# Optimization experiments

Measured on AMD Instinct MI355X. Metric: run time of the kernel, lower is better.

Reference implementation:

```python
import jax, jax.numpy as jnp
import numpy as np

B, DIM, H, W = 2, 48, 256, 256
HEADS = 8
CHEAD = DIM // HEADS
HID = int(DIM * 2)


def _conv2d(x, w, stride=1, pad=0, dil=1, groups=1):
    return jax.lax.conv_general_dilated(
        x, w, (stride, stride), [(pad, pad), (pad, pad)],
        rhs_dilation=(dil, dil), feature_group_count=groups,
        dimension_numbers=('NCHW', 'OIHW', 'NCHW'))


def _ln(x, w, b):
    # WithBias LayerNorm over the channel axis (to_3d makes channels the last dim)
    mu = jnp.mean(x, axis=1, keepdims=True)
    var = jnp.mean((x - mu) ** 2, axis=1, keepdims=True)
    return (x - mu) / jnp.sqrt(var + 1e-5) * w[None, :, None, None] + b[None, :, None, None]


def _gelu(x):
    return jax.nn.gelu(x, approximate=False)


def setup_inputs() -> dict:
    key = jax.random.key(0)
    ks = iter(jax.random.split(key, 40))
    nrm = lambda *s: jax.random.normal(next(ks), s, dtype=jnp.float32) * 0.02
    d = dict(
        x=jax.random.normal(next(ks), (B, DIM, H, W), dtype=jnp.float32),
        ln1_w=jnp.ones(DIM), ln1_b=jnp.zeros(DIM),
        qkv_w=nrm(3 * DIM, DIM),            # 1x1x1 Conv3d == channel linear
        qkv_dw_w=nrm(3 * DIM, 1, 3, 3),     # center depth slice of 3x3x3 depthwise (depth=1 input)
        proj_w=nrm(DIM, DIM),
        fc_w=nrm(9, 3 * HEADS), fc_b=jnp.zeros(9),
        dep_w=nrm(DIM, 9, 3, 3), dep_b=jnp.zeros(DIM),  # groups = dim//heads
        l2q_w=nrm(DIM, DIM), l2q_b=jnp.zeros(DIM),
        temperature=jnp.ones(HEADS),
        ln2_w=jnp.ones(DIM), ln2_b=jnp.zeros(DIM),
        pin_w=nrm(3 * HID, DIM),
        dw1_w=nrm(HID, 1, 3, 3), dw2_w=nrm(HID, 1, 3, 3), dw3_w=nrm(HID, 1, 3, 3),
        pout_w=nrm(DIM, HID),
    )
    for i in range(3):
        d[f'cv_w{i}'] = nrm(DIM, DIM, 3, 3)
        d[f'cv_b{i}'] = jnp.zeros(DIM)
        d[f'cln_w{i}'] = jnp.ones(DIM)
        d[f'cln_b{i}'] = jnp.zeros(DIM)
    return d


def _forward(x, ln1_w, ln1_b, qkv_w, qkv_dw_w, proj_w, fc_w, fc_b, dep_w, dep_b,
             l2q_w, l2q_b, temperature, ln2_w, ln2_b, pin_w, dw1_w, dw2_w, dw3_w,
             pout_w, cv_w0, cv_b0, cln_w0, cln_b0, cv_w1, cv_b1, cln_w1, cln_b1,
             cv_w2, cv_b2, cln_w2, cln_b2):
    b, c, h, w = x.shape
    heads = temperature.shape[0]
    chead = c // heads

    # ---- Conv2DTransformer branch -> pooled descriptor x_d [b, c]
    t = x
    for cw, cb, lw, lb in ((cv_w0, cv_b0, cln_w0, cln_b0),
                           (cv_w1, cv_b1, cln_w1, cln_b1),
                           (cv_w2, cv_b2, cln_w2, cln_b2)):
        t = _conv2d(t, cw, stride=2, pad=1) + cb[None, :, None, None]
        t = jax.nn.relu(_ln(t, lw, lb))
        t = jax.lax.reduce_window(t, -jnp.inf, jax.lax.max, (1, 1, 2, 2), (1, 1, 2, 2), 'VALID')
    x_d = _gelu(jnp.mean(t, axis=(2, 3)))  # [b, c]

    # ---- Attention
    xn = _ln(x, ln1_w, ln1_b)
    qkv = jnp.einsum('oc,bchw->bohw', qkv_w, xn)
    qkv = _conv2d(qkv, qkv_dw_w, pad=1, groups=3 * c)  # depthwise, [b,3c,h,w]

    # conv-attention path: raw-memory reshape exactly as torch .reshape
    f_all = qkv.reshape(b, h * w, 3 * heads, chead).transpose(0, 2, 1, 3)  # [b,3H,hw,chead]
    f_all = jnp.einsum('oi,bipc->bopc', fc_w, f_all) + fc_b[None, :, None, None]  # [b,9,hw,chead]
    f_conv = f_all.transpose(0, 3, 1, 2).reshape(b, 9 * chead, h, w)
    out_conv = _conv2d(f_conv, dep_w, pad=1, groups=chead) + dep_b[None, :, None, None]

    # outer-product bias from pooled descriptor
    q0 = (x_d @ l2q_w.T + l2q_b).reshape(b, heads, chead)
    q0m = q0[:, :, :, None] * q0[:, :, None, :]  # [b,head,chead,chead]

    q, k, v = jnp.split(qkv, 3, axis=1)
    rs = lambda t_: t_.reshape(b, heads, chead, h * w)
    q, k, v = rs(q), rs(k), rs(v)
    nz = lambda t_: t_ / jnp.maximum(jnp.linalg.norm(t_, axis=-1, keepdims=True), 1e-12)
    q, k = nz(q), nz(k)

    attn = jnp.einsum('bhcx,bhdx->bhcd', q, k) * temperature[None, :, None, None]
    attn = jax.nn.softmax(attn * q0m, axis=-1)
    out = jnp.einsum('bhcd,bhdx->bhcx', attn, v).reshape(b, c, h, w)
    out = jnp.einsum('oc,bchw->bohw', proj_w, out) + out_conv

    x = x + out

    # ---- FeedForward (3-branch dilated depthwise)
    xn2 = _ln(x, ln2_w, ln2_b)
    y = jnp.einsum('oc,bchw->bohw', pin_w, xn2)  # [b,3*hid,h,w]
    hid = y.shape[1] // 3
    y1, y2, y3 = jnp.split(y, 3, axis=1)
    y1 = _conv2d(y1, dw1_w, pad=1, groups=hid)
    y2 = _conv2d(y2, dw2_w, pad=2, dil=2, groups=hid)
    y3 = _conv2d(y3, dw3_w, pad=3, dil=3, groups=hid)
    y = _gelu(y1) * y2 * y3
    return x + jnp.einsum('oc,bchw->bohw', pout_w, y)


def reference(x, ln1_w, ln1_b, qkv_w, qkv_dw_w, proj_w, fc_w, fc_b, dep_w, dep_b,
              l2q_w, l2q_b, temperature, ln2_w, ln2_b, pin_w, dw1_w, dw2_w, dw3_w,
              pout_w, cv_w0, cv_b0, cln_w0, cln_b0, cv_w1, cv_b1, cln_w1, cln_b1,
              cv_w2, cv_b2, cln_w2, cln_b2):
    return _forward(x, ln1_w, ln1_b, qkv_w, qkv_dw_w, proj_w, fc_w, fc_b, dep_w, dep_b,
                    l2q_w, l2q_b, temperature, ln2_w, ln2_b, pin_w, dw1_w, dw2_w, dw3_w,
                    pout_w, cv_w0, cv_b0, cln_w0, cln_b0, cv_w1, cv_b1, cln_w1, cln_b1,
                    cv_w2, cv_b2, cln_w2, cln_b2)
```

## Files before the change

kernel.cpp:

```cpp
#include <hip/hip_runtime.h>

constexpr int NB = 2;
constexpr int NC = 48;
constexpr int NH = 256;
constexpr int NW = 256;
constexpr int NP = NH * NW;
constexpr int NHEADS = 8;
constexpr int NCHD = 6;
constexpr int NHID = 96;
constexpr int GSEG = 64;

typedef unsigned short bf16_t;
typedef __attribute__((ext_vector_type(8))) short bf16x8;
typedef __attribute__((ext_vector_type(4))) float f32x4;

__device__ __forceinline__ float bf2f(bf16_t u) {
  union { unsigned int i; float f; } c; c.i = ((unsigned int)u) << 16; return c.f;
}
__device__ __forceinline__ bf16_t f2bf(float f) {
  union { float f; unsigned int i; } c; c.f = f;
  unsigned int r = (c.i + 0x7FFFu + ((c.i >> 16) & 1u)) >> 16;
  return (bf16_t)r;
}
__device__ __forceinline__ void unpack2(unsigned int u, float& a, float& b) {
  union { unsigned int i; float f; } c0, c1;
  c0.i = u << 16; c1.i = u & 0xffff0000u;
  a = c0.f; b = c1.f;
}

__device__ __forceinline__ float gelu_f(float v) {
  float u = v * (0.79788456f + 0.0356774081f * v * v);
  u = fminf(fmaxf(u, -9.f), 9.f);
  float e = __expf(-2.f * u);
  float th = (1.f - e) / (1.f + e);
  return 0.5f * v * (1.f + th);
}

#define STENCIL_ROW(LROW, D, WVAL0, WVAL1, WVAL2, ACC)                        \
  {                                                                            \
    const float* lp = &lds[(LROW) * 272 + quad * 4];                           \
    float4 va = *(const float4*)lp;                                            \
    float4 vb = *(const float4*)(lp + 4);                                      \
    float4 vc = *(const float4*)(lp + 8);                                      \
    float v[12] = {va.x, va.y, va.z, va.w, vb.x, vb.y, vb.z, vb.w,             \
                   vc.x, vc.y, vc.z, vc.w};                                    \
    _Pragma("unroll") for (int jj = 0; jj < 4; ++jj) {                         \
      ACC[jj] = fmaf(v[jj - (D) + 4], WVAL0, ACC[jj]);                         \
      ACC[jj] = fmaf(v[jj + 4], WVAL1, ACC[jj]);                               \
      ACC[jj] = fmaf(v[jj + (D) + 4], WVAL2, ACC[jj]);                         \
    }                                                                          \
  }

__global__ __launch_bounds__(512) void k_conv_s2_tile(const float* __restrict__ in,
                                                      const float* __restrict__ w,
                                                      const float* __restrict__ bias,
                                                      float* __restrict__ out,
                                                      int IH, int IW, int OH, int OW) {
  __shared__ float lds[16 * 442];
  int tilesX = OW >> 3;
  int tilesY = OH >> 3;
  int blk = blockIdx.x;
  int tx = blk % tilesX;
  int t = blk / tilesX;
  int ty = t % tilesY;
  int b = t / tilesY;
  int oy0 = ty * 8, ox0 = tx * 8;
  int iy0 = oy0 * 2 - 1, ix0 = ox0 * 2 - 1;
  const float* inb = in + (size_t)b * NC * IH * IW;

  int lane = threadIdx.x & 63;
  int oy = lane >> 3, ox = lane & 7;
  int ocb = __builtin_amdgcn_readfirstlane((threadIdx.x >> 6) * 6);
  float acc[6];
  #pragma unroll
  for (int j = 0; j < 6; ++j) acc[j] = bias[ocb + j];
  int rbase = oy * 52;

  for (int chunk = 0; chunk < 3; ++chunk) {
    int icb = chunk * 16;
    for (int i = threadIdx.x; i < 16 * 17 * 17; i += 512) {
      int cc = i % 17;
      int t2 = i / 17;
      int rr = t2 % 17;
      int ic = t2 / 17;
      float v = 0.f;
      int iy = iy0 + rr, ix = ix0 + cc;
      if ((unsigned)iy < (unsigned)IH && (unsigned)ix < (unsigned)IW)
        v = inb[((size_t)(icb + ic) * IH + iy) * IW + ix];
      lds[ic * 442 + rr * 26 + ((cc & 1) ? 13 + (cc >> 1) : (cc >> 1))] = v;
    }
    __syncthreads();

    for (int ic16 = 0; ic16 < 16; ++ic16) {
      const float* base = lds + ic16 * 442 + rbase;
      float e0[3], e1[3], ov[3];
      #pragma unroll
      for (int ky = 0; ky < 3; ++ky) {
        const float* rowp = base + ky * 26;
        e0[ky] = rowp[ox];
        e1[ky] = rowp[ox + 1];
        ov[ky] = rowp[13 + ox];
      }
      const float* wpc = w + (size_t)(ocb * 48 + icb + ic16) * 9;
      #pragma unroll
      for (int j = 0; j < 6; ++j) {
        const float* wp = wpc + (size_t)j * 48 * 9;
        float a = acc[j];
        #pragma unroll
        for (int ky = 0; ky < 3; ++ky) {
          a = fmaf(wp[ky * 3 + 0], e0[ky], a);
          a = fmaf(wp[ky * 3 + 1], ov[ky], a);
          a = fmaf(wp[ky * 3 + 2], e1[ky], a);
        }
        acc[j] = a;
      }
    }
    __syncthreads();
  }

  float* ob = out + (size_t)b * NC * OH * OW;
  #pragma unroll
  for (int j = 0; j < 6; ++j)
    ob[((size_t)(ocb + j) * OH + oy0 + oy) * OW + ox0 + ox] = acc[j];
}

__global__ void k_lnpool(const float* __restrict__ in, const float* __restrict__ lw,
                         const float* __restrict__ lb, float* __restrict__ out,
                         int IH, int IW) {
  int OH = IH >> 1, OW = IW >> 1;
  int idx = blockIdx.x * blockDim.x + threadIdx.x;
  int total = NB * OH * OW;
  if (idx >= total) return;
  int ox = idx % OW;
  int t = idx / OW;
  int oy = t % OH;
  int b = t / OH;
  const float* inb = in + (size_t)b * NC * IH * IW;
  float mu[4], rs[4];
  #pragma unroll
  for (int q = 0; q < 4; ++q) {
    int iy = oy * 2 + (q >> 1), ix = ox * 2 + (q & 1);
    float s = 0.f, ss = 0.f;
    for (int c = 0; c < NC; ++c) {
      float v = inb[((size_t)c * IH + iy) * IW + ix];
      s += v; ss += v * v;
    }
    float m = s * (1.f / NC);
    mu[q] = m;
    rs[q] = rsqrtf(fmaxf(ss * (1.f / NC) - m * m, 0.f) + 1e-5f);
  }
  for (int c = 0; c < NC; ++c) {
    float best = 0.f;
    float wv = lw[c], bv = lb[c];
    #pragma unroll
    for (int q = 0; q < 4; ++q) {
      int iy = oy * 2 + (q >> 1), ix = ox * 2 + (q & 1);
      float v = inb[((size_t)c * IH + iy) * IW + ix];
      v = (v - mu[q]) * rs[q] * wv + bv;
      best = fmaxf(best, fmaxf(v, 0.f));
    }
    out[((size_t)(b * NC + c) * OH + oy) * OW + ox] = best;
  }
}

__global__ void k_head(const float* __restrict__ p3, const float* __restrict__ l2qw,
                       const float* __restrict__ l2qb, float* __restrict__ q0m) {
  __shared__ float xd[NC], q0[NC];
  int b = blockIdx.x, t = threadIdx.x;
  if (t < NC) {
    float s = 0.f;
    for (int i = 0; i < 16; ++i) s += p3[(b * NC + t) * 16 + i];
    xd[t] = gelu_f(s * (1.f / 16.f));
  }
  __syncthreads();
  if (t < NC) {
    float a = l2qb[t];
    for (int c = 0; c < NC; ++c) a += xd[c] * l2qw[t * NC + c];
    q0[t] = a;
  }
  __syncthreads();
  if (t < NHEADS * NCHD * NCHD) {
    int h = t / 36, r = t % 36, c = r / 6, d = r % 6;
    q0m[b * 288 + t] = q0[h * 6 + c] * q0[h * 6 + d];
  }
}

__global__ void k_prep(const float* __restrict__ qkvw, const float* __restrict__ ln1w,
                       const float* __restrict__ ln1b, const float* __restrict__ pinw,
                       const float* __restrict__ ln2w, const float* __restrict__ ln2b,
                       const float* __restrict__ poutw, const float* __restrict__ projw,
                       float* __restrict__ SB, bf16_t* __restrict__ WA1,
                       bf16_t* __restrict__ WA2, bf16_t* __restrict__ WP,
                       bf16_t* __restrict__ WJ) {
  int t = blockIdx.x * blockDim.x + threadIdx.x;
  int stride = gridDim.x * blockDim.x;
  if (t < 144) {
    float s = 0.f, bb = 0.f;
    for (int c = 0; c < 48; ++c) {
      float w = qkvw[t * 48 + c];
      s = fmaf(w, ln1w[c], s); bb = fmaf(w, ln1b[c], bb);
    }
    SB[t] = s; SB[144 + t] = bb;
  } else if (t < 144 + 288) {
    int o = t - 144;
    float s = 0.f, bb = 0.f;
    for (int c = 0; c < 48; ++c) {
      float w = pinw[o * 48 + c];
      s = fmaf(w, ln2w[c], s); bb = fmaf(w, ln2b[c], bb);
    }
    SB[288 + o] = s; SB[576 + o] = bb;
  }
  for (int i = t; i < 9 * 1024; i += stride) {
    int j = i & 7, lane = (i >> 3) & 63, s = (i >> 9) & 1, ot = i >> 10;
    int o = ot * 16 + (lane & 15);
    int k = s * 32 + ((lane >> 4) << 3) + j;
    float v = (k < 48) ? qkvw[o * 48 + k] * ln1w[k] : 0.f;
    WA1[i] = f2bf(v);
  }
  for (int i = t; i < 18 * 1024; i += stride) {
    int j = i & 7, lane = (i >> 3) & 63, s = (i >> 9) & 1, ot = i >> 10;
    int o = ot * 16 + (lane & 15);
    int k = s * 32 + ((lane >> 4) << 3) + j;
    float v = (k < 48) ? pinw[o * 48 + k] * ln2w[k] : 0.f;
    WA2[i] = f2bf(v);
  }
  for (int i = t; i < 9 * 512; i += stride) {
    int j = i & 7, lane = (i >> 3) & 63;
    int fi = i >> 9;
    int s = fi % 3, ot = fi / 3;
    int o = ot * 16 + (lane & 15);
    int k = s * 32 + ((lane >> 4) << 3) + j;
    WP[i] = f2bf(poutw[o * 96 + k]);
  }
  for (int i = t; i < 6 * 512; i += stride) {
    int j = i & 7, lane = (i >> 3) & 63;
    int fi = i >> 9;
    int s = fi & 1, ot = fi >> 1;
    int o = ot * 16 + (lane & 15);
    int k = s * 32 + ((lane >> 4) << 3) + j;
    float v = (k < 48) ? projw[o * 48 + k] : 0.f;
    WJ[i] = f2bf(v);
  }
}

__global__ __launch_bounds__(256) void k_chmix_mfma(const float* __restrict__ x,
                                                    const bf16_t* __restrict__ WA,
                                                    const float* __restrict__ S,
                                                    const float* __restrict__ Bc,
                                                    bf16_t* __restrict__ out,
                                                    int nout) {
  __shared__ bf16_t xT[64 * 72];
  __shared__ float smu[64], srstd[64];
  int blk = blockIdx.x;
  int pxt = blk & 1023;
  int b = blk >> 10;
  int pbase = pxt * 64;
  const float* xb = x + (size_t)b * NC * NP + pbase;
  int p4 = threadIdx.x & 15, k0 = threadIdx.x >> 4;
  #pragma unroll
  for (int it = 0; it < 3; ++it) {
    int k = k0 + it * 16;
    float4 v = *(const float4*)(xb + (size_t)k * NP + p4 * 4);
    xT[(p4 * 4 + 0) * 72 + k] = f2bf(v.x);
    xT[(p4 * 4 + 1) * 72 + k] = f2bf(v.y);
    xT[(p4 * 4 + 2) * 72 + k] = f2bf(v.z);
    xT[(p4 * 4 + 3) * 72 + k] = f2bf(v.w);
  }
  {
    int k = 48 + k0;
    xT[(p4 * 4 + 0) * 72 + k] = 0;
    xT[(p4 * 4 + 1) * 72 + k] = 0;
    xT[(p4 * 4 + 2) * 72 + k] = 0;
    xT[(p4 * 4 + 3) * 72 + k] = 0;
  }
  __syncthreads();
  if (threadIdx.x < 64) {
    int t = threadIdx.x;
    float s = 0.f, ss = 0.f;
    #pragma unroll
    for (int k4 = 0; k4 < 12; ++k4) {
      ushort4 u = *(const ushort4*)&xT[t * 72 + k4 * 4];
      float a0 = bf2f(u.x), a1 = bf2f(u.y), a2 = bf2f(u.z), a3 = bf2f(u.w);
      s += a0 + a1 + a2 + a3;
      ss = fmaf(a0, a0, ss); ss = fmaf(a1, a1, ss);
      ss = fmaf(a2, a2, ss); ss = fmaf(a3, a3, ss);
    }
    float mu = s * (1.f / NC);
    smu[t] = mu;
    srstd[t] = rsqrtf(fmaxf(ss * (1.f / NC) - mu * mu, 0.f) + 1e-5f);
  }
  int w = threadIdx.x >> 6;
  int lane = threadIdx.x & 63;
  bf16x8 bfr0 = *(const bf16x8*)&xT[(w * 16 + (lane & 15)) * 72 + ((lane >> 4) << 3)];
  bf16x8 bfr1 = *(const bf16x8*)&xT[(w * 16 + (lane & 15)) * 72 + 32 + ((lane >> 4) << 3)];
  __syncthreads();
  float mu = smu[w * 16 + (lane & 15)];
  float rs = srstd[w * 16 + (lane & 15)];
  int p = pbase + w * 16 + (lane & 15);
  int nt = nout >> 4;
  bf16_t* ob = out + (size_t)b * nout * NP + p;
  for (int ot = 0; ot < nt; ++ot) {
    bf16x8 a0 = *(const bf16x8*)(WA + (size_t)(ot * 2 + 0) * 512 + lane * 8);
    bf16x8 a1 = *(const bf16x8*)(WA + (size_t)(ot * 2 + 1) * 512 + lane * 8);
    f32x4 acc = {0.f, 0.f, 0.f, 0.f};
    acc = __builtin_amdgcn_mfma_f32_16x16x32_bf16(a0, bfr0, acc, 0, 0, 0);
    acc = __builtin_amdgcn_mfma_f32_16x16x32_bf16(a1, bfr1, acc, 0, 0, 0);
    int orow = ot * 16 + ((lane >> 4) << 2);
    #pragma unroll
    for (int j = 0; j < 4; ++j) {
      int o = orow + j;
      float r = fmaf(rs, acc[j] - mu * S[o], Bc[o]);
      ob[(size_t)o * NP] = f2bf(r);
    }
  }
}

__global__ __launch_bounds__(256) void k_dw144(const bf16_t* __restrict__ in,
                                               const float* __restrict__ w9,
                                               bf16_t* __restrict__ out) {
  __shared__ float lds[6 * 272];
  int blk = blockIdx.x;
  int rq = blk & 63;
  int ch = (blk >> 6) % 144;
  int b = blk / (144 * 64);
  int yy0 = rq * 4;
  const bf16_t* ib = in + (size_t)(b * 144 + ch) * NP;
  for (int i = threadIdx.x; i < 6 * 68; i += 256) {
    int sr = i / 68, c4 = i % 68;
    int iy = yy0 + sr - 1;
    float4 v = make_float4(0.f, 0.f, 0.f, 0.f);
    if ((unsigned)iy < (unsigned)NH && c4 >= 1 && c4 <= 64) {
      ushort4 u = *(const ushort4*)(ib + iy * NW + (c4 - 1) * 4);
      v = make_float4(bf2f(u.x), bf2f(u.y), bf2f(u.z), bf2f(u.w));
    }
    *(float4*)(&lds[sr * 272 + c4 * 4]) = v;
  }
  __syncthreads();
  int q = threadIdx.x >> 6;
  int quad = threadIdx.x & 63;
  const float* wp = w9 + ch * 9;
  float acc[4] = {0.f, 0.f, 0.f, 0.f};
  #pragma unroll
  for (int rr = 0; rr < 3; ++rr)
    STENCIL_ROW(q + rr, 1, wp[rr * 3 + 0], wp[rr * 3 + 1], wp[rr * 3 + 2], acc);
  *(ushort4*)(out + (size_t)(b * 144 + ch) * NP + (yy0 + q) * NW + quad * 4) =
      make_ushort4(f2bf(acc[0]), f2bf(acc[1]), f2bf(acc[2]), f2bf(acc[3]));
}

__global__ __launch_bounds__(256) void k_gram(const bf16_t* __restrict__ qkvd,
                                              float* __restrict__ spart) {
  int gid = blockIdx.x;
  int seg = gid & (GSEG - 1), h = (gid >> 6) & 7, b = gid >> 9;
  const bf16_t* qb = qkvd + (size_t)(b * 144 + h * 6) * NP;
  const bf16_t* kb = qkvd + (size_t)(b * 144 + 48 + h * 6) * NP;
  float acc[48];
  #pragma unroll
  for (int j = 0; j < 48; ++j) acc[j] = 0.f;
  int p0 = seg * (NP / GSEG) + threadIdx.x * 4;
  float qv[6][4], kv[6][4];
  #pragma unroll
  for (int c = 0; c < 6; ++c) {
    ushort4 uq = *(const ushort4*)(qb + (size_t)c * NP + p0);
    qv[c][0] = bf2f(uq.x); qv[c][1] = bf2f(uq.y); qv[c][2] = bf2f(uq.z); qv[c][3] = bf2f(uq.w);
    ushort4 uk = *(const ushort4*)(kb + (size_t)c * NP + p0);
    kv[c][0] = bf2f(uk.x); kv[c][1] = bf2f(uk.y); kv[c][2] = bf2f(uk.z); kv[c][3] = bf2f(uk.w);
  }
  #pragma unroll
  for (int px = 0; px < 4; ++px) {
    #pragma unroll
    for (int c = 0; c < 6; ++c)
      #pragma unroll
      for (int d = 0; d < 6; ++d)
        acc[c * 6 + d] = fmaf(qv[c][px], kv[d][px], acc[c * 6 + d]);
    #pragma unroll
    for (int c = 0; c < 6; ++c) acc[36 + c] = fmaf(qv[c][px], qv[c][px], acc[36 + c]);
    #pragma unroll
    for (int d = 0; d < 6; ++d) acc[42 + d] = fmaf(kv[d][px], kv[d][px], acc[42 + d]);
  }
  int lane = threadIdx.x & 63, wid = threadIdx.x >> 6;
  __shared__ float sr[4 * 48];
  #pragma unroll
  for (int j = 0; j < 48; ++j) {
    float v = acc[j];
    #pragma unroll
    for (int off = 32; off; off >>= 1) v += __shfl_down(v, off, 64);
    if (lane == 0) sr[wid * 48 + j] = v;
  }
  __syncthreads();
  if (threadIdx.x < 48)
    spart[(size_t)gid * 48 + threadIdx.x] =
        sr[threadIdx.x] + sr[48 + threadIdx.x] + sr[96 + threadIdx.x] + sr[144 + threadIdx.x];
}

__global__ __launch_bounds__(256) void k_attn(const float* __restrict__ spart,
                                              const float* __restrict__ temp,
                                              const float* __restrict__ q0m,
                                              float* __restrict__ A) {
  int b = blockIdx.x;
  __shared__ float tot[8 * 48];
  for (int j = threadIdx.x; j < 384; j += 256) {
    int h = j / 48, v = j % 48;
    const float* base = spart + ((size_t)(b * 8 + h) * GSEG) * 48 + v;
    float s = 0.f;
    for (int seg = 0; seg < GSEG; ++seg) s += base[(size_t)seg * 48];
    tot[j] = s;
  }
  __syncthreads();
  int t = threadIdx.x;
  if (t >= 48) return;
  int h = t / 6, c = t % 6;
  const float* T = &tot[h * 48];
  float nq = fmaxf(sqrtf(T[36 + c]), 1e-12f);
  float tm = temp[h];
  float lg[6];
  #pragma unroll
  for (int d = 0; d < 6; ++d) {
    float nk = fmaxf(sqrtf(T[42 + d]), 1e-12f);
    lg[d] = (T[c * 6 + d] / (nq * nk)) * tm * q0m[b * 288 + h * 36 + c * 6 + d];
  }
  float m = lg[0];
  #pragma unroll
  for (int d = 1; d < 6; ++d) m = fmaxf(m, lg[d]);
  float sum = 0.f;
  #pragma unroll
  for (int d = 0; d < 6; ++d) { lg[d] = expf(lg[d] - m); sum += lg[d]; }
  float inv = 1.f / sum;
  #pragma unroll
  for (int d = 0; d < 6; ++d) A[b * 288 + h * 36 + c * 6 + d] = lg[d] * inv;
}

__global__ __launch_bounds__(384) void k_fc(const bf16_t* __restrict__ qkvd,
                                            const float* __restrict__ fcw,
                                            const float* __restrict__ fcb,
                                            bf16_t* __restrict__ fconv) {
  __shared__ float sin_[9216];
  __shared__ float sout[3456];
  int blk = blockIdx.x;
  int b = blk >> 10, p0 = (blk & 1023) << 6;
  const bf16_t* src = qkvd + (size_t)b * 144 * NP + (size_t)p0 * 144;
  const uint4* src4 = (const uint4*)src;
  for (int i = threadIdx.x; i < 1152; i += 384) {
    uint4 u = src4[i];
    float* d = &sin_[i * 8];
    unpack2(u.x, d[0], d[1]);
    unpack2(u.y, d[2], d[3]);
    unpack2(u.z, d[4], d[5]);
    unpack2(u.w, d[6], d[7]);
  }
  __syncthreads();
  int pl = threadIdx.x / 6, c2 = threadIdx.x % 6;
  float xv[24];
  #pragma unroll
  for (int g = 0; g < 24; ++g) xv[g] = sin_[pl * 144 + g * 6 + c2];
  #pragma unroll
  for (int o = 0; o < 9; ++o) {
    float a = fcb[o];
    #pragma unroll
    for (int g = 0; g < 24; ++g) a += fcw[o * 24 + g] * xv[g];
    sout[(c2 * 9 + o) * 64 + pl] = a;
  }
  __syncthreads();
  for (int i = threadIdx.x; i < 1728; i += 384) {
    int ch = i >> 5, pr = (i & 31) * 2;
    *(ushort2*)(fconv + (size_t)(b * 54 + ch) * NP + p0 + pr) =
        make_ushort2(f2bf(sout[ch * 64 + pr]), f2bf(sout[ch * 64 + pr + 1]));
  }
}

__global__ __launch_bounds__(256, 4) void k_depconv(const bf16_t* __restrict__ fconv,
                                                    const float* __restrict__ dw,
                                                    const float* __restrict__ db,
                                                    bf16_t* __restrict__ outconv) {
  __shared__ bf16_t lds16[9 * 6 * 272];
  int blk = blockIdx.x;
  int rq = blk & 63;
  int g = (blk >> 6) % 6;
  int b = blk / (6 * 64);
  int yy0 = rq * 4;
  const bf16_t* fb = fconv + (size_t)(b * 54 + g * 9) * NP;
  for (int i = threadIdx.x; i < 9 * 6 * 68; i += 256) {
    int j = i / 408;
    int rem = i % 408;
    int sr = rem / 68, c4 = rem % 68;
    int iy = yy0 + sr - 1;
    ushort4 v = make_ushort4(0, 0, 0, 0);
    if ((unsigned)iy < (unsigned)NH && c4 >= 1 && c4 <= 64)
      v = *(const ushort4*)(fb + (size_t)j * NP + iy * NW + (c4 - 1) * 4);
    *(ushort4*)(&lds16[(j * 6 + sr) * 272 + c4 * 4]) = v;
  }
  __syncthreads();
  int q = threadIdx.x >> 6;
  int quad = threadIdx.x & 63;
  float acc[8][4];
  #pragma unroll
  for (int o = 0; o < 8; ++o) {
    float bv = db[g * 8 + o];
    #pragma unroll
    for (int jj = 0; jj < 4; ++jj) acc[o][jj] = bv;
  }
  const float* wg = dw + (size_t)(g * 8) * 81;
  #pragma unroll
  for (int j = 0; j < 9; ++j) {
    #pragma unroll
    for (int rr = 0; rr < 3; ++rr) {
      const bf16_t* lp = &lds16[((j * 6) + q + rr) * 272 + quad * 4];
      ushort4 ua = *(const ushort4*)lp;
      ushort4 ub = *(const ushort4*)(lp + 4);
      ushort4 uc = *(const ushort4*)(lp + 8);
      float v[12] = {bf2f(ua.x), bf2f(ua.y), bf2f(ua.z), bf2f(ua.w),
                     bf2f(ub.x), bf2f(ub.y), bf2f(ub.z), bf2f(ub.w),
                     bf2f(uc.x), bf2f(uc.y), bf2f(uc.z), bf2f(uc.w)};
      #pragma unroll
      for (int dxi = 0; dxi < 3; ++dxi) {
        int wi = j * 9 + rr * 3 + dxi;
        #pragma unroll
        for (int o = 0; o < 8; ++o) {
          float wv = wg[o * 81 + wi];
          #pragma unroll
          for (int jj = 0; jj < 4; ++jj)
            acc[o][jj] = fmaf(v[jj + dxi + 3], wv, acc[o][jj]);
        }
      }
    }
  }
  bf16_t* ob = outconv + ((size_t)(b * NC + g * 8) * NH + yy0 + q) * NW + quad * 4;
  #pragma unroll
  for (int o = 0; o < 8; ++o)
    *(ushort4*)(ob + (size_t)o * NP) =
        make_ushort4(f2bf(acc[o][0]), f2bf(acc[o][1]), f2bf(acc[o][2]), f2bf(acc[o][3]));
}

__global__ __launch_bounds__(256) void k_proj_mfma(const bf16_t* __restrict__ qkvd,
                                                   const float* __restrict__ A,
                                                   const bf16_t* __restrict__ WJ,
                                                   const float* __restrict__ x,
                                                   const bf16_t* __restrict__ outconv,
                                                   float* __restrict__ x1) {
  __shared__ bf16_t vT[64 * 72];
  __shared__ bf16_t avT[64 * 72];
  __shared__ float sA[288];
  int blk = blockIdx.x;
  int pxt = blk & 1023;
  int b = blk >> 10;
  int pbase = pxt * 64;
  const bf16_t* vb = qkvd + (size_t)(b * 144 + 96) * NP + pbase;
  int p4 = threadIdx.x & 15, k0 = threadIdx.x >> 4;
  #pragma unroll
  for (int it = 0; it < 3; ++it) {
    int k = k0 + it * 16;
    ushort4 u = *(const ushort4*)(vb + (size_t)k * NP + p4 * 4);
    vT[(p4 * 4 + 0) * 72 + k] = u.x;
    vT[(p4 * 4 + 1) * 72 + k] = u.y;
    vT[(p4 * 4 + 2) * 72 + k] = u.z;
    vT[(p4 * 4 + 3) * 72 + k] = u.w;
  }
  {
    int k = 48 + k0;
    avT[(p4 * 4 + 0) * 72 + k] = 0;
    avT[(p4 * 4 + 1) * 72 + k] = 0;
    avT[(p4 * 4 + 2) * 72 + k] = 0;
    avT[(p4 * 4 + 3) * 72 + k] = 0;
  }
  for (int i = threadIdx.x; i < 288; i += 256) sA[i] = A[b * 288 + i];
  __syncthreads();
  {
    int px = threadIdx.x & 63, hh = threadIdx.x >> 6;
    #pragma unroll
    for (int hi = 0; hi < 2; ++hi) {
      int h = hh * 2 + hi;
      float v6[6];
      #pragma unroll
      for (int d = 0; d < 6; ++d) v6[d] = bf2f(vT[px * 72 + h * 6 + d]);
      #pragma unroll
      for (int c = 0; c < 6; ++c) {
        float av = 0.f;
        #pragma unroll
        for (int d = 0; d < 6; ++d) av = fmaf(sA[h * 36 + c * 6 + d], v6[d], av);
        avT[px * 72 + h * 6 + c] = f2bf(av);
      }
    }
  }
  __syncthreads();
  int w = threadIdx.x >> 6;
  int lane = threadIdx.x & 63;
  int prow = w * 16 + (lane & 15);
  bf16x8 f0 = *(const bf16x8*)&avT[prow * 72 + ((lane >> 4) << 3)];
  bf16x8 f1 = *(const bf16x8*)&avT[prow * 72 + 32 + ((lane >> 4) << 3)];
  int p = pbase + prow;
  const float* xb = x + (size_t)b * NC * NP + p;
  const bf16_t* ob = outconv + (size_t)b * NC * NP + p;
  float* x1b = x1 + (size_t)b * NC * NP + p;
  #pragma unroll
  for (int ot = 0; ot < 3; ++ot) {
    bf16x8 a0 = *(const bf16x8*)(WJ + (size_t)(ot * 2 + 0) * 512 + lane * 8);
    bf16x8 a1 = *(const bf16x8*)(WJ + (size_t)(ot * 2 + 1) * 512 + lane * 8);
    f32x4 acc = {0.f, 0.f, 0.f, 0.f};
    acc = __builtin_amdgcn_mfma_f32_16x16x32_bf16(a0, f0, acc, 0, 0, 0);
    acc = __builtin_amdgcn_mfma_f32_16x16x32_bf16(a1, f1, acc, 0, 0, 0);
    int orow = ot * 16 + ((lane >> 4) << 2);
    #pragma unroll
    for (int j = 0; j < 4; ++j) {
      int o = orow + j;
      x1b[(size_t)o * NP] = xb[(size_t)o * NP] + acc[j] + bf2f(ob[(size_t)o * NP]);
    }
  }
}

__global__ __launch_bounds__(256) void k_ffdw(const bf16_t* __restrict__ y,
                                              const float* __restrict__ w1,
                                              const float* __restrict__ w2,
                                              const float* __restrict__ w3,
                                              bf16_t* __restrict__ z) {
  __shared__ float lds[24 * 272];
  int blk = blockIdx.x;
  int rq = blk & 63;
  int ch = (blk >> 6) % NHID;
  int b = blk / (NHID * 64);
  int yy0 = rq * 4;
  const bf16_t* yb = y + (size_t)(b * 288 + ch) * NP;
  if (threadIdx.x < 96) {
    int sr = threadIdx.x >> 2, part = threadIdx.x & 3;
    int slot = (part == 0) ? 0 : (256 + part * 4);
    *(float4*)(&lds[sr * 272 + slot]) = make_float4(0.f, 0.f, 0.f, 0.f);
  }
  #pragma unroll
  for (int it = 0; it < 6; ++it) {
    int sr = (threadIdx.x >> 6) + it * 4;
    int m = threadIdx.x & 63;
    int br, iy;
    if (sr < 6)       { br = 0; iy = yy0 + sr - 1; }
    else if (sr < 14) { br = 1; iy = yy0 + sr - 8; }
    else              { br = 2; iy = yy0 + sr - 17; }
    float4 v = make_float4(0.f, 0.f, 0.f, 0.f);
    if ((unsigned)iy < (unsigned)NH) {
      ushort4 u = *(const ushort4*)(yb + (size_t)(br * NHID) * NP + iy * NW + m * 4);
      v = make_float4(bf2f(u.x), bf2f(u.y), bf2f(u.z), bf2f(u.w));
    }
    *(float4*)(&lds[sr * 272 + 4 + m * 4]) = v;
  }
  __syncthreads();
  int q = threadIdx.x >> 6;
  int quad = threadIdx.x & 63;
  const float* wp1 = w1 + ch * 9;
  const float* wp2 = w2 + ch * 9;
  const float* wp3 = w3 + ch * 9;
  float c1[4] = {0.f, 0.f, 0.f, 0.f};
  float c2[4] = {0.f, 0.f, 0.f, 0.f};
  float c3[4] = {0.f, 0.f, 0.f, 0.f};
  #pragma unroll
  for (int rr = 0; rr < 3; ++rr)
    STENCIL_ROW(0 + q + rr * 1, 1, wp1[rr * 3 + 0], wp1[rr * 3 + 1], wp1[rr * 3 + 2], c1);
  #pragma unroll
  for (int rr = 0; rr < 3; ++rr)
    STENCIL_ROW(6 + q + rr * 2, 2, wp2[rr * 3 + 0], wp2[rr * 3 + 1], wp2[rr * 3 + 2], c2);
  #pragma unroll
  for (int rr = 0; rr < 3; ++rr)
    STENCIL_ROW(14 + q + rr * 3, 3, wp3[rr * 3 + 0], wp3[rr * 3 + 1], wp3[rr * 3 + 2], c3);
  *(ushort4*)(z + (size_t)(b * NHID + ch) * NP + (yy0 + q) * NW + quad * 4) =
      make_ushort4(f2bf(gelu_f(c1[0]) * c2[0] * c3[0]),
                   f2bf(gelu_f(c1[1]) * c2[1] * c3[1]),
                   f2bf(gelu_f(c1[2]) * c2[2] * c3[2]),
                   f2bf(gelu_f(c1[3]) * c2[3] * c3[3]));
}

__global__ __launch_bounds__(256) void k_pout_mfma(const bf16_t* __restrict__ z,
                                                   const bf16_t* __restrict__ WP,
                                                   const float* __restrict__ x1,
                                                   float* __restrict__ outp) {
  __shared__ bf16_t zT[64 * 104];
  int blk = blockIdx.x;
  int pxt = blk & 1023;
  int b = blk >> 10;
  int pbase = pxt * 64;
  const bf16_t* zb = z + (size_t)b * NHID * NP + pbase;
  int p4 = threadIdx.x & 15, k0 = threadIdx.x >> 4;
  #pragma unroll
  for (int it = 0; it < 6; ++it) {
    int k = k0 + it * 16;
    ushort4 u = *(const ushort4*)(zb + (size_t)k * NP + p4 * 4);
    zT[(p4 * 4 + 0) * 104 + k] = u.x;
    zT[(p4 * 4 + 1) * 104 + k] = u.y;
    zT[(p4 * 4 + 2) * 104 + k] = u.z;
    zT[(p4 * 4 + 3) * 104 + k] = u.w;
  }
  __syncthreads();
  int w = threadIdx.x >> 6;
  int lane = threadIdx.x & 63;
  int prow = w * 16 + (lane & 15);
  bf16x8 bfr[3];
  #pragma unroll
  for (int s = 0; s < 3; ++s)
    bfr[s] = *(const bf16x8*)&zT[prow * 104 + s * 32 + ((lane >> 4) << 3)];
  int p = pbase + prow;
  const float* x1b = x1 + (size_t)b * NC * NP + p;
  float* ob = outp + (size_t)b * NC * NP + p;
  #pragma unroll
  for (int ot = 0; ot < 3; ++ot) {
    f32x4 acc = {0.f, 0.f, 0.f, 0.f};
    #pragma unroll
    for (int s = 0; s < 3; ++s) {
      bf16x8 a = *(const bf16x8*)(WP + (size_t)(ot * 3 + s) * 512 + lane * 8);
      acc = __builtin_amdgcn_mfma_f32_16x16x32_bf16(a, bfr[s], acc, 0, 0, 0);
    }
    int orow = ot * 16 + ((lane >> 4) << 2);
    #pragma unroll
    for (int j = 0; j < 4; ++j) {
      int o = orow + j;
      ob[(size_t)o * NP] = x1b[(size_t)o * NP] + acc[j];
    }
  }
}

constexpr size_t SZ_QKV = (size_t)NB * 144 * NP;
constexpr size_t SZ_CHW = (size_t)NB * NC * NP;
constexpr size_t OFF_QKV0 = 0;
constexpr size_t OFF_QKVD = OFF_QKV0 + SZ_QKV;
constexpr size_t OFF_FCONV = OFF_QKVD + SZ_QKV;
constexpr size_t SZ_FCONV = (size_t)NB * 54 * NP;
constexpr size_t OFF_OUTCONV = OFF_FCONV + SZ_FCONV;
constexpr size_t OFF_X1 = OFF_OUTCONV + SZ_CHW;
constexpr size_t OFF_STATS = OFF_X1 + SZ_CHW;
constexpr size_t OFF_T1 = OFF_STATS + (size_t)NB * NP * 2;
constexpr size_t OFF_P1 = OFF_T1 + (size_t)NB * NC * 128 * 128;
constexpr size_t OFF_T2 = OFF_P1 + (size_t)NB * NC * 64 * 64;
constexpr size_t OFF_P2 = OFF_T2 + (size_t)NB * NC * 32 * 32;
constexpr size_t OFF_T3 = OFF_P2 + (size_t)NB * NC * 16 * 16;
constexpr size_t OFF_P3 = OFF_T3 + (size_t)NB * NC * 8 * 8;
constexpr size_t OFF_Q0M = OFF_P3 + (size_t)NB * NC * 4 * 4;
constexpr size_t OFF_NORMS = OFF_Q0M + 576;
constexpr size_t OFF_SPART = OFF_NORMS + 192;
constexpr size_t OFF_A = OFF_SPART + (size_t)NB * 64 * 48;

extern "C" void kernel_launch(void* const* d_in, const int* in_sizes, int n_in,
                              void* d_out, int out_size, void* d_ws, size_t ws_size,
                              hipStream_t stream) {
  const float* x     = (const float*)d_in[0];
  const float* ln1w  = (const float*)d_in[1];
  const float* ln1b  = (const float*)d_in[2];
  const float* qkvw  = (const float*)d_in[3];
  const float* qkvdw = (const float*)d_in[4];
  const float* projw = (const float*)d_in[5];
  const float* fcw   = (const float*)d_in[6];
  const float* fcb   = (const float*)d_in[7];
  const float* depw  = (const float*)d_in[8];
  const float* depb  = (const float*)d_in[9];
  const float* l2qw  = (const float*)d_in[10];
  const float* l2qb  = (const float*)d_in[11];
  const float* temp  = (const float*)d_in[12];
  const float* ln2w  = (const float*)d_in[13];
  const float* ln2b  = (const float*)d_in[14];
  const float* pinw  = (const float*)d_in[15];
  const float* dw1   = (const float*)d_in[16];
  const float* dw2   = (const float*)d_in[17];
  const float* dw3   = (const float*)d_in[18];
  const float* poutw = (const float*)d_in[19];
  const float* cvw0  = (const float*)d_in[20];
  const float* cvb0  = (const float*)d_in[21];
  const float* clw0  = (const float*)d_in[22];
  const float* clb0  = (const float*)d_in[23];
  const float* cvw1  = (const float*)d_in[24];
  const float* cvb1  = (const float*)d_in[25];
  const float* clw1  = (const float*)d_in[26];
  const float* clb1  = (const float*)d_in[27];
  const float* cvw2  = (const float*)d_in[28];
  const float* cvb2  = (const float*)d_in[29];
  const float* clw2  = (const float*)d_in[30];
  const float* clb2  = (const float*)d_in[31];

  float* ws = (float*)d_ws;
  bf16_t* qkv0 = (bf16_t*)(ws + OFF_QKV0);
  bf16_t* qkvd = (bf16_t*)(ws + OFF_QKVD);
  bf16_t* fconv = (bf16_t*)(ws + OFF_FCONV);
  bf16_t* outconv = (bf16_t*)(ws + OFF_OUTCONV);
  float* x1 = ws + OFF_X1;
  float* t1 = ws + OFF_T1;
  float* p1 = ws + OFF_P1;
  float* t2 = ws + OFF_T2;
  float* p2 = ws + OFF_P2;
  float* t3 = ws + OFF_T3;
  float* p3 = ws + OFF_P3;
  float* q0m = ws + OFF_Q0M;
  float* spart = ws + OFF_STATS;
  float* A = ws + OFF_SPART;
  float* SB = ws + OFF_T1;
  bf16_t* WA1 = (bf16_t*)(ws + OFF_T1 + 1024);
  bf16_t* WA2 = (bf16_t*)(ws + OFF_T1 + 1024 + 4608);
  bf16_t* WP  = (bf16_t*)(ws + OFF_T1 + 1024 + 4608 + 9216);
  bf16_t* WJ  = (bf16_t*)(ws + OFF_T1 + 1024 + 4608 + 9216 + 2304);
  bf16_t* ybuf = (bf16_t*)(ws + OFF_QKV0);
  bf16_t* zbuf = (bf16_t*)(ws + OFF_FCONV);

  k_conv_s2_tile<<<512, 512, 0, stream>>>(x, cvw0, cvb0, t1, 256, 256, 128, 128);
  k_lnpool<<<32, 256, 0, stream>>>(t1, clw0, clb0, p1, 128, 128);
  k_conv_s2_tile<<<32, 512, 0, stream>>>(p1, cvw1, cvb1, t2, 64, 64, 32, 32);
  k_lnpool<<<2, 256, 0, stream>>>(t2, clw1, clb1, p2, 32, 32);
  k_conv_s2_tile<<<2, 512, 0, stream>>>(p2, cvw2, cvb2, t3, 16, 16, 8, 8);
  k_lnpool<<<1, 256, 0, stream>>>(t3, clw2, clb2, p3, 8, 8);
  k_head<<<2, 320, 0, stream>>>(p3, l2qw, l2qb, q0m);

  k_prep<<<8, 256, 0, stream>>>(qkvw, ln1w, ln1b, pinw, ln2w, ln2b, poutw, projw,
                                SB, WA1, WA2, WP, WJ);

  k_chmix_mfma<<<NB * 1024, 256, 0, stream>>>(x, WA1, SB, SB + 144, qkv0, 144);
  k_dw144<<<NB * 144 * 64, 256, 0, stream>>>(qkv0, qkvdw, qkvd);
  k_gram<<<NB * NHEADS * GSEG, 256, 0, stream>>>(qkvd, spart);
  k_attn<<<2, 256, 0, stream>>>(spart, temp, q0m, A);
  k_fc<<<2048, 384, 0, stream>>>(qkvd, fcw, fcb, fconv);
  k_depconv<<<768, 256, 0, stream>>>(fconv, depw, depb, outconv);
  k_proj_mfma<<<NB * 1024, 256, 0, stream>>>(qkvd, A, WJ, x, outconv, x1);

  k_chmix_mfma<<<NB * 1024, 256, 0, stream>>>(x1, WA2, SB + 288, SB + 576, ybuf, 288);
  k_ffdw<<<NB * NHID * 64, 256, 0, stream>>>(ybuf, dw1, dw2, dw3, zbuf);
  k_pout_mfma<<<NB * 1024, 256, 0, stream>>>(zbuf, WP, x1, (float*)d_out);
}
```

Measured before the change: 383.1 us.

## Run first stride-2 3x3 conv on MFMA bf16 with prepacked weights

```diff
diff --git a/kernel.cpp b/kernel.cpp
--- a/kernel.cpp
+++ b/kernel.cpp
@@ -50,6 +50,88 @@
       ACC[jj] = fmaf(v[jj + (D) + 4], WVAL2, ACC[jj]);                         \
     }                                                                          \
   }
+
+__global__ void k_prepw(const float* __restrict__ cvw0, bf16_t* __restrict__ WC) {
+  int i = blockIdx.x * blockDim.x + threadIdx.x;
+  if (i >= 9 * 3 * 2 * 512) return;
+  int j = i & 7, lane = (i >> 3) & 63;
+  int fi = i >> 9;
+  int s = fi & 1;
+  int tot = fi >> 1;
+  int ot = tot % 3, t = tot / 3;
+  int o = ot * 16 + (lane & 15);
+  int k = s * 32 + ((lane >> 4) << 3) + j;
+  float v = (k < 48) ? cvw0[(size_t)(o * 48 + k) * 9 + t] : 0.f;
+  WC[i] = f2bf(v);
+}
+
+__global__ __launch_bounds__(512) void k_conv1_mfma(const float* __restrict__ in,
+                                                    const bf16_t* __restrict__ WC,
+                                                    const float* __restrict__ bias,
+                                                    float* __restrict__ out) {
+  __shared__ bf16_t xs[17 * 17 * 72];
+  __shared__ float red[4 * 3 * 64 * 4];
+  int blk = blockIdx.x;
+  int tx = blk & 15;
+  int t0 = blk >> 4;
+  int ty = t0 & 15, b = t0 >> 4;
+  int oy0 = ty * 8, ox0 = tx * 8;
+  int iy0 = oy0 * 2 - 1, ix0 = ox0 * 2 - 1;
+  const float* inb = in + (size_t)b * NC * NP;
+  for (int i = threadIdx.x; i < 17 * 17 * 48; i += 512) {
+    int cc = i % 17;
+    int t2 = i / 17;
+    int rr = t2 % 17;
+    int ic = t2 / 17;
+    float v = 0.f;
+    int iy = iy0 + rr, ix = ix0 + cc;
+    if ((unsigned)iy < 256u && (unsigned)ix < 256u)
+      v = inb[((size_t)ic << 16) + (iy << 8) + ix];
+    xs[(rr * 17 + cc) * 72 + ic] = f2bf(v);
+  }
+  for (int i = threadIdx.x; i < 289 * 16; i += 512) {
+    int rcc = i >> 4, icz = i & 15;
+    xs[rcc * 72 + 48 + icz] = 0;
+  }
+  __syncthreads();
+  int wid = threadIdx.x >> 6, lane = threadIdx.x & 63;
+  int pt = wid & 3, s = wid >> 2;
+  int l15 = lane & 15, kl = lane >> 4;
+  int px = pt * 16 + l15;
+  int oy = px >> 3, ox = px & 7;
+  int base = ((oy * 2) * 17 + ox * 2) * 72 + s * 32 + kl * 8;
+  f32x4 acc[3] = {{0.f, 0.f, 0.f, 0.f}, {0.f, 0.f, 0.f, 0.f}, {0.f, 0.f, 0.f, 0.f}};
+  #pragma unroll
+  for (int t = 0; t < 9; ++t) {
+    int dy = t / 3, dx = t % 3;
+    bf16x8 bf = *(const bf16x8*)&xs[base + dy * (17 * 72) + dx * 72];
+    #pragma unroll
+    for (int ot = 0; ot < 3; ++ot) {
+      bf16x8 af = *(const bf16x8*)(WC + (size_t)((t * 3 + ot) * 2 + s) * 512 + lane * 8);
+      acc[ot] = __builtin_amdgcn_mfma_f32_16x16x32_bf16(af, bf, acc[ot], 0, 0, 0);
+    }
+  }
+  if (s == 1) {
+    #pragma unroll
+    for (int ot = 0; ot < 3; ++ot)
+      #pragma unroll
+      for (int j = 0; j < 4; ++j)
+        red[((pt * 3 + ot) * 64 + lane) * 4 + j] = acc[ot][j];
+  }
+  __syncthreads();
+  if (s == 0) {
+    float* ob = out + (size_t)b * NC * 16384;
+    #pragma unroll
+    for (int ot = 0; ot < 3; ++ot) {
+      #pragma unroll
+      for (int j = 0; j < 4; ++j) {
+        int o = ot * 16 + kl * 4 + j;
+        float r = acc[ot][j] + red[((pt * 3 + ot) * 64 + lane) * 4 + j] + bias[o];
+        ob[((size_t)o * 128 + oy0 + oy) * 128 + ox0 + ox] = r;
+      }
+    }
+  }
+}
 
 __global__ __launch_bounds__(512) void k_conv_s2_tile(const float* __restrict__ in,
                                                       const float* __restrict__ w,
@@ -787,10 +869,12 @@
   bf16_t* WA2 = (bf16_t*)(ws + OFF_T1 + 1024 + 4608);
   bf16_t* WP  = (bf16_t*)(ws + OFF_T1 + 1024 + 4608 + 9216);
   bf16_t* WJ  = (bf16_t*)(ws + OFF_T1 + 1024 + 4608 + 9216 + 2304);
+  bf16_t* WC = (bf16_t*)(ws + OFF_QKV0);
   bf16_t* ybuf = (bf16_t*)(ws + OFF_QKV0);
   bf16_t* zbuf = (bf16_t*)(ws + OFF_FCONV);
 
-  k_conv_s2_tile<<<512, 512, 0, stream>>>(x, cvw0, cvb0, t1, 256, 256, 128, 128);
+  k_prepw<<<108, 256, 0, stream>>>(cvw0, WC);
+  k_conv1_mfma<<<512, 512, 0, stream>>>(x, WC, cvb0, t1);
   k_lnpool<<<32, 256, 0, stream>>>(t1, clw0, clb0, p1, 128, 128);
   k_conv_s2_tile<<<32, 512, 0, stream>>>(p1, cvw1, cvb1, t2, 64, 64, 32, 32);
   k_lnpool<<<2, 256, 0, stream>>>(t2, clw1, clb1, p2, 32, 32);
```

After: 369.5 us. 3.6% less time.
